# Optimization experiments

Hardware: AMD Instinct MI355X
Metric: run time of the kernel (lower is better)

The kernel has to match this reference:

```python
import jax, jax.numpy as jnp
import numpy as np

E, W, D = 50000, 6, 512
NH = 8
HD = D // NH
EPS = 1e-6


def setup_inputs() -> dict:
    key = jax.random.key(0)
    ks = jax.random.split(key, 12)
    s = 1.0 / np.sqrt(D)
    s2 = 1.0 / np.sqrt(D // 2)
    return {
        "h_i": jax.random.normal(ks[0], (E, D), jnp.float32),
        "evo_j": jax.random.normal(ks[1], (E, W, D), jnp.float32),
        "var_i": jax.random.uniform(ks[2], (E, D), jnp.float32),
        "var_j": jax.random.uniform(ks[3], (E, D), jnp.float32),
        "Wq": jax.random.normal(ks[4], (D, D), jnp.float32) * s,
        "bq": jnp.zeros((D,), jnp.float32),
        "Wk": jax.random.normal(ks[5], (D, D), jnp.float32) * s,
        "bk": jnp.zeros((D,), jnp.float32),
        "Wv": jax.random.normal(ks[6], (D, D), jnp.float32) * s,
        "bv": jnp.zeros((D,), jnp.float32),
        "log_decay": jnp.asarray(-2.0, jnp.float32),
        "W1": jax.random.normal(ks[7], (D, D // 2), jnp.float32) * s,
        "b1": jnp.zeros((D // 2,), jnp.float32),
        "W2": jax.random.normal(ks[8], (D // 2, 1), jnp.float32) * s2,
        "b2": jnp.zeros((1,), jnp.float32),
    }


def reference(h_i, evo_j, var_i, var_j, Wq, bq, Wk, bk, Wv, bv, log_decay, W1, b1, W2, b2):
    E_, W_, D_ = evo_j.shape
    scale = HD ** (-0.5)
    # projections: [E, nh, hd] and [E, W, nh, hd]
    Q = (h_i @ Wq + bq).reshape(E_, NH, HD)
    K = (evo_j @ Wk + bk).reshape(E_, W_, NH, HD)
    V = (evo_j @ Wv + bv).reshape(E_, W_, NH, HD)
    # windowed attention scores [E, nh, W]
    scores = jnp.einsum("ehd,ewhd->ehw", Q, K) * scale
    steps = jnp.arange(W_, dtype=jnp.float32)
    decay_w = jnp.exp(jnp.exp(log_decay) * steps)
    scores = scores + (decay_w / decay_w.sum())[None, None, :]
    attn = jax.nn.softmax(scores, axis=-1)
    # pool V over the window: [E, nh, hd] -> [E, D]
    pooled = jnp.einsum("ehw,ewhd->ehd", attn, V).reshape(E_, D_)
    # trust head: Linear -> GELU(exact) -> Linear
    hmid = jax.nn.gelu(pooled @ W1 + b1, approximate=False)
    trust_logit = (hmid @ W2 + b2)[:, 0]
    conf_i = 1.0 / (1.0 + jnp.maximum(jnp.sqrt(var_i.mean(-1)), EPS))
    conf_j = 1.0 / (1.0 + jnp.maximum(jnp.sqrt(var_j.mean(-1)), EPS))
    conf = jnp.sqrt(conf_i * conf_j)
    return jax.nn.sigmoid(trust_logit + jnp.maximum(jnp.log(conf), -5.0))
```

## Files before the change

kernel.cpp:

```cpp
#include <hip/hip_runtime.h>
#include <hip/hip_fp16.h>

typedef _Float16 f16;
typedef _Float16 f16x8 __attribute__((ext_vector_type(8)));
typedef __fp16 fp16x2_raw __attribute__((ext_vector_type(2)));
typedef float f32x4 __attribute__((ext_vector_type(4)));

#define DD 512
#define BM 32
#define WW 6
#define NH 8
#define QS 520
#define ES 136
#define EMAX 50000

union F16x8 { f16x8 v; unsigned u[4]; uint2 u2[2]; };
union H2U { __half2 h; unsigned u; };
union U4H { uint4 q; __half2 h[4]; };

__device__ __forceinline__ unsigned pkrtz(float a, float b) {
  union { fp16x2_raw h; unsigned u; } c;
  c.h = __builtin_amdgcn_cvt_pkrtz(a, b);
  return c.u;
}
__device__ __forceinline__ unsigned short f2h(float x) {
  union { f16 h; unsigned short u; } c; c.h = (f16)x; return c.u;
}
__device__ __forceinline__ float gelu_fast(float x) {
  float u = __expf(1.5957691216f * (x + 0.044715f * x * x * x));
  return x * u / (u + 1.f);
}
#define SCHED_FENCE() __builtin_amdgcn_sched_barrier(0)

__global__ void k_prep_qv(const float* __restrict__ src, unsigned short* __restrict__ dst) {
  int i = blockIdx.x * 256 + threadIdx.x;
  int j0 = (i & 1) * 4;
  int lane = (i >> 1) & 63;
  int kst = (i >> 7) & 15;
  int ct = (i >> 11) & 3;
  int wv = (i >> 13) & 7;
  int col = wv * 64 + ct * 16 + (lane & 15);
  int row = kst * 32 + (lane >> 4) * 8 + j0;
  ushort4 o;
  o.x = f2h(src[(size_t)(row + 0) * DD + col]);
  o.y = f2h(src[(size_t)(row + 1) * DD + col]);
  o.z = f2h(src[(size_t)(row + 2) * DD + col]);
  o.w = f2h(src[(size_t)(row + 3) * DD + col]);
  *(ushort4*)&dst[(size_t)(((wv * 4 + ct) * 16 + kst) * 64 + lane) * 8 + j0] = o;
}

__global__ void k_prep_wk(const float* __restrict__ src, unsigned short* __restrict__ dst) {
  int i = blockIdx.x * 256 + threadIdx.x;
  int j0 = (i & 1) * 4;
  int lane = (i >> 1) & 63;
  int ab = (i >> 7) & 1;
  int kst = (i >> 8) & 1;
  int ch = (i >> 9) & 15;
  int wv = (i >> 13) & 7;
  int row = ch * 32 + ab * 16 + (lane & 15);
  int cb = wv * 64 + kst * 32 + (j0 ? 16 : 0) + ((lane >> 4) & 3) * 4;
  float4 v = *(const float4*)&src[(size_t)row * DD + cb];
  ushort4 o; o.x = f2h(v.x); o.y = f2h(v.y); o.z = f2h(v.z); o.w = f2h(v.w);
  *(ushort4*)&dst[(size_t)((((wv * 16 + ch) * 2 + kst) * 2 + ab) * 64 + lane) * 8 + j0] = o;
}

__global__ void k_prep_w1(const float* __restrict__ src, unsigned short* __restrict__ dst) {
  int i = blockIdx.x * 256 + threadIdx.x;
  int j0 = (i & 1) * 4;
  int lane = (i >> 1) & 63;
  int kst = (i >> 7) & 15;
  int ct = (i >> 11) & 1;
  int wv = (i >> 12) & 7;
  int col = wv * 32 + ct * 16 + (lane & 15);
  int row = kst * 32 + (lane >> 4) * 8 + j0;
  ushort4 o;
  o.x = f2h(src[(size_t)(row + 0) * 256 + col]);
  o.y = f2h(src[(size_t)(row + 1) * 256 + col]);
  o.z = f2h(src[(size_t)(row + 2) * 256 + col]);
  o.w = f2h(src[(size_t)(row + 3) * 256 + col]);
  *(ushort4*)&dst[(size_t)(((wv * 2 + ct) * 16 + kst) * 64 + lane) * 8 + j0] = o;
}

__global__ __launch_bounds__(512, 4) void trust_main(
    const float* __restrict__ h_i, const float* __restrict__ evo,
    const float* __restrict__ var_i, const float* __restrict__ var_j,
    const float* __restrict__ bq, const float* __restrict__ bk, const float* __restrict__ bv,
    const float* __restrict__ ld, const float* __restrict__ b1,
    const float* __restrict__ W2, const float* __restrict__ b2,
    const unsigned short* __restrict__ wqA, const unsigned short* __restrict__ wkA,
    const unsigned short* __restrict__ wvA, const unsigned short* __restrict__ w1A,
    float* __restrict__ out) {
  __shared__ unsigned short buf_s[192 * ES];
  __shared__ float score_s[NH * BM * WW];
  __shared__ float logit_s[BM * NH];
  __shared__ float conf_s[BM];

  unsigned short* qh_s = buf_s;
  unsigned short* evo_s = buf_s;

  const int t = threadIdx.x;
  const int wv = t >> 6;
  const int l = t & 63;
  const int l16 = l & 15;
  const int lq = l >> 4;
  const int e0 = blockIdx.x * BM;
  const int row6 = e0 * 6;

  const float4* evb = (const float4*)evo;

  {
    const float4* h4 = (const float4*)h_i;
    #pragma unroll 4
    for (int i = 0; i < 8; ++i) {
      int idx = i * 512 + t;
      int row = idx >> 7, c4 = idx & 127;
      int ee = e0 + row; if (ee > EMAX - 1) ee = EMAX - 1;
      float4 v = h4[(size_t)ee * 128 + c4];
      uint2 o; o.x = pkrtz(v.x, v.y); o.y = pkrtz(v.z, v.w);
      *(uint2*)&qh_s[row * QS + c4 * 4] = o;
    }
    int ce = t >> 4, cs = t & 15;
    int ee = e0 + ce; if (ee > EMAX - 1) ee = EMAX - 1;
    const float4* vi4 = (const float4*)var_i + (size_t)ee * 128;
    const float4* vj4 = (const float4*)var_j + (size_t)ee * 128;
    float si = 0.f, sj = 0.f;
    #pragma unroll 4
    for (int i = 0; i < 8; ++i) {
      float4 a = vi4[i * 16 + cs]; si += a.x + a.y + a.z + a.w;
      float4 b = vj4[i * 16 + cs]; sj += b.x + b.y + b.z + b.w;
    }
    #pragma unroll
    for (int m = 1; m <= 8; m <<= 1) { si += __shfl_xor(si, m); sj += __shfl_xor(sj, m); }
    if (cs == 0) {
      float ci = 1.f / (1.f + fmaxf(sqrtf(si * (1.f / DD)), 1e-6f));
      float cj = 1.f / (1.f + fmaxf(sqrtf(sj * (1.f / DD)), 1e-6f));
      conf_s[ce] = fmaxf(0.5f * (__logf(ci) + __logf(cj)), -5.0f);
    }
  }
  __syncthreads();
  SCHED_FENCE();

  F16x8 qfrA[2], qfrB[2];
  float qbA, qbB;
  {
    f32x4 qaccA[4] = {}, qaccB[4] = {};
    const unsigned short* wqp = wqA + (size_t)wv * 4 * 16 * 512 + l * 8;
    #pragma unroll 2
    for (int kst = 0; kst < 16; ++kst) {
      f16x8 hbA = *reinterpret_cast<const f16x8*>(&qh_s[l16 * QS + kst * 32 + lq * 8]);
      f16x8 hbB = *reinterpret_cast<const f16x8*>(&qh_s[(16 + l16) * QS + kst * 32 + lq * 8]);
      #pragma unroll
      for (int ct = 0; ct < 4; ++ct) {
        f16x8 a = *reinterpret_cast<const f16x8*>(&wqp[(ct * 16 + kst) * 512]);
        qaccA[ct] = __builtin_amdgcn_mfma_f32_16x16x32_f16(a, hbA, qaccA[ct], 0, 0, 0);
        qaccB[ct] = __builtin_amdgcn_mfma_f32_16x16x32_f16(a, hbB, qaccB[ct], 0, 0, 0);
      }
    }
    qbA = 0.f; qbB = 0.f;
    #pragma unroll
    for (int ct = 0; ct < 4; ++ct) {
      float4 bq4 = *(const float4*)&bq[wv * 64 + ct * 16 + lq * 4];
      float4 bk4 = *(const float4*)&bk[wv * 64 + ct * 16 + lq * 4];
      {
        float q0 = qaccA[ct][0] + bq4.x, q1 = qaccA[ct][1] + bq4.y;
        float q2 = qaccA[ct][2] + bq4.z, q3 = qaccA[ct][3] + bq4.w;
        qbA += q0 * bk4.x + q1 * bk4.y + q2 * bk4.z + q3 * bk4.w;
        qfrA[ct >> 1].u[(ct & 1) * 2]     = pkrtz(q0, q1);
        qfrA[ct >> 1].u[(ct & 1) * 2 + 1] = pkrtz(q2, q3);
      }
      {
        float q0 = qaccB[ct][0] + bq4.x, q1 = qaccB[ct][1] + bq4.y;
        float q2 = qaccB[ct][2] + bq4.z, q3 = qaccB[ct][3] + bq4.w;
        qbB += q0 * bk4.x + q1 * bk4.y + q2 * bk4.z + q3 * bk4.w;
        qfrB[ct >> 1].u[(ct & 1) * 2]     = pkrtz(q0, q1);
        qfrB[ct >> 1].u[(ct & 1) * 2 + 1] = pkrtz(q2, q3);
      }
    }
    qbA += __shfl_xor(qbA, 16); qbA += __shfl_xor(qbA, 32);
    qbB += __shfl_xor(qbB, 16); qbB += __shfl_xor(qbB, 32);
  }
  SCHED_FENCE();

  f32x4 sA0 = {}, sA1 = {}, sA2 = {}, sA3 = {}, sA4 = {}, sA5 = {};
  f32x4 sB0 = {}, sB1 = {}, sB2 = {}, sB3 = {}, sB4 = {}, sB5 = {};
  const unsigned short* wkp = wkA + (size_t)wv * 16 * 2 * 2 * 512 + l * 8;
  const unsigned short* wvp = wvA + (size_t)wv * 4 * 16 * 512 + l * 8;

  #pragma unroll 1
  for (int q = 0; q < 4; ++q) {
    __syncthreads();
    #pragma unroll 4
    for (int i = 0; i < 12; ++i) {
      int idx = i * 512 + t;
      int row = idx >> 5, c4 = idx & 31;
      int gr = row6 + row; if (gr > EMAX * 6 - 1) gr = EMAX * 6 - 1;
      float4 v = evb[(size_t)gr * 128 + q * 32 + c4];
      uint2 o; o.x = pkrtz(v.x, v.y); o.y = pkrtz(v.z, v.w);
      *(uint2*)&evo_s[row * ES + c4 * 4] = o;
    }
    __syncthreads();
    #pragma unroll 1
    for (int ci = 0; ci < 4; ++ci) {
      int ch = q * 4 + ci;
      F16x8 a00, a01, a10, a11;
      a00.v = *reinterpret_cast<const f16x8*>(&wkp[((ch * 2 + 0) * 2 + 0) * 512]);
      a01.v = *reinterpret_cast<const f16x8*>(&wkp[((ch * 2 + 0) * 2 + 1) * 512]);
      a10.v = *reinterpret_cast<const f16x8*>(&wkp[((ch * 2 + 1) * 2 + 0) * 512]);
      a11.v = *reinterpret_cast<const f16x8*>(&wkp[((ch * 2 + 1) * 2 + 1) * 512]);
      SCHED_FENCE();
      f32x4 qkA0 = {}, qkA1 = {}, qkB0 = {}, qkB1 = {};
      qkA0 = __builtin_amdgcn_mfma_f32_16x16x32_f16(a00.v, qfrA[0].v, qkA0, 0, 0, 0);
      qkA1 = __builtin_amdgcn_mfma_f32_16x16x32_f16(a01.v, qfrA[0].v, qkA1, 0, 0, 0);
      qkB0 = __builtin_amdgcn_mfma_f32_16x16x32_f16(a00.v, qfrB[0].v, qkB0, 0, 0, 0);
      qkB1 = __builtin_amdgcn_mfma_f32_16x16x32_f16(a01.v, qfrB[0].v, qkB1, 0, 0, 0);
      qkA0 = __builtin_amdgcn_mfma_f32_16x16x32_f16(a10.v, qfrA[1].v, qkA0, 0, 0, 0);
      qkA1 = __builtin_amdgcn_mfma_f32_16x16x32_f16(a11.v, qfrA[1].v, qkA1, 0, 0, 0);
      qkB0 = __builtin_amdgcn_mfma_f32_16x16x32_f16(a10.v, qfrB[1].v, qkB0, 0, 0, 0);
      qkB1 = __builtin_amdgcn_mfma_f32_16x16x32_f16(a11.v, qfrB[1].v, qkB1, 0, 0, 0);
      F16x8 afA, afB;
      afA.u[0] = pkrtz(qkA0[0], qkA0[1]); afA.u[1] = pkrtz(qkA0[2], qkA0[3]);
      afA.u[2] = pkrtz(qkA1[0], qkA1[1]); afA.u[3] = pkrtz(qkA1[2], qkA1[3]);
      afB.u[0] = pkrtz(qkB0[0], qkB0[1]); afB.u[1] = pkrtz(qkB0[2], qkB0[3]);
      afB.u[2] = pkrtz(qkB1[0], qkB1[1]); afB.u[3] = pkrtz(qkB1[2], qkB1[3]);
      int cb = ci * 32 + lq * 4;
      F16x8 b;
      b.u2[0] = *(const uint2*)&evo_s[(0 * 16 + l16) * ES + cb];
      b.u2[1] = *(const uint2*)&evo_s[(0 * 16 + l16) * ES + cb + 16];
      sA0 = __builtin_amdgcn_mfma_f32_16x16x32_f16(afA.v, b.v, sA0, 0, 0, 0);
      b.u2[0] = *(const uint2*)&evo_s[(1 * 16 + l16) * ES + cb];
      b.u2[1] = *(const uint2*)&evo_s[(1 * 16 + l16) * ES + cb + 16];
      sA1 = __builtin_amdgcn_mfma_f32_16x16x32_f16(afA.v, b.v, sA1, 0, 0, 0);
      b.u2[0] = *(const uint2*)&evo_s[(2 * 16 + l16) * ES + cb];
      b.u2[1] = *(const uint2*)&evo_s[(2 * 16 + l16) * ES + cb + 16];
      sA2 = __builtin_amdgcn_mfma_f32_16x16x32_f16(afA.v, b.v, sA2, 0, 0, 0);
      b.u2[0] = *(const uint2*)&evo_s[(3 * 16 + l16) * ES + cb];
      b.u2[1] = *(const uint2*)&evo_s[(3 * 16 + l16) * ES + cb + 16];
      sA3 = __builtin_amdgcn_mfma_f32_16x16x32_f16(afA.v, b.v, sA3, 0, 0, 0);
      b.u2[0] = *(const uint2*)&evo_s[(4 * 16 + l16) * ES + cb];
      b.u2[1] = *(const uint2*)&evo_s[(4 * 16 + l16) * ES + cb + 16];
      sA4 = __builtin_amdgcn_mfma_f32_16x16x32_f16(afA.v, b.v, sA4, 0, 0, 0);
      b.u2[0] = *(const uint2*)&evo_s[(5 * 16 + l16) * ES + cb];
      b.u2[1] = *(const uint2*)&evo_s[(5 * 16 + l16) * ES + cb + 16];
      sA5 = __builtin_amdgcn_mfma_f32_16x16x32_f16(afA.v, b.v, sA5, 0, 0, 0);
      b.u2[0] = *(const uint2*)&evo_s[(6 * 16 + l16) * ES + cb];
      b.u2[1] = *(const uint2*)&evo_s[(6 * 16 + l16) * ES + cb + 16];
      sB0 = __builtin_amdgcn_mfma_f32_16x16x32_f16(afB.v, b.v, sB0, 0, 0, 0);
      b.u2[0] = *(const uint2*)&evo_s[(7 * 16 + l16) * ES + cb];
      b.u2[1] = *(const uint2*)&evo_s[(7 * 16 + l16) * ES + cb + 16];
      sB1 = __builtin_amdgcn_mfma_f32_16x16x32_f16(afB.v, b.v, sB1, 0, 0, 0);
      b.u2[0] = *(const uint2*)&evo_s[(8 * 16 + l16) * ES + cb];
      b.u2[1] = *(const uint2*)&evo_s[(8 * 16 + l16) * ES + cb + 16];
      sB2 = __builtin_amdgcn_mfma_f32_16x16x32_f16(afB.v, b.v, sB2, 0, 0, 0);
      b.u2[0] = *(const uint2*)&evo_s[(9 * 16 + l16) * ES + cb];
      b.u2[1] = *(const uint2*)&evo_s[(9 * 16 + l16) * ES + cb + 16];
      sB3 = __builtin_amdgcn_mfma_f32_16x16x32_f16(afB.v, b.v, sB3, 0, 0, 0);
      b.u2[0] = *(const uint2*)&evo_s[(10 * 16 + l16) * ES + cb];
      b.u2[1] = *(const uint2*)&evo_s[(10 * 16 + l16) * ES + cb + 16];
      sB4 = __builtin_amdgcn_mfma_f32_16x16x32_f16(afB.v, b.v, sB4, 0, 0, 0);
      b.u2[0] = *(const uint2*)&evo_s[(11 * 16 + l16) * ES + cb];
      b.u2[1] = *(const uint2*)&evo_s[(11 * 16 + l16) * ES + cb + 16];
      sB5 = __builtin_amdgcn_mfma_f32_16x16x32_f16(afB.v, b.v, sB5, 0, 0, 0);
    }
  }
  SCHED_FENCE();

  #pragma unroll
  for (int r = 0; r < 4; ++r) {
    int e = lq * 4 + r;
    int base = l16 - 6 * e;
    { int w = base;      if (w >= 0 && w < WW) { score_s[wv * 192 + e * 6 + w] = sA0[r];
                                                score_s[wv * 192 + (16 + e) * 6 + w] = sB0[r]; } }
    { int w = base + 16; if (w >= 0 && w < WW) { score_s[wv * 192 + e * 6 + w] = sA1[r];
                                                score_s[wv * 192 + (16 + e) * 6 + w] = sB1[r]; } }
    { int w = base + 32; if (w >= 0 && w < WW) { score_s[wv * 192 + e * 6 + w] = sA2[r];
                                                score_s[wv * 192 + (16 + e) * 6 + w] = sB2[r]; } }
    { int w = base + 48; if (w >= 0 && w < WW) { score_s[wv * 192 + e * 6 + w] = sA3[r];
                                                score_s[wv * 192 + (16 + e) * 6 + w] = sB3[r]; } }
    { int w = base + 64; if (w >= 0 && w < WW) { score_s[wv * 192 + e * 6 + w] = sA4[r];
                                                score_s[wv * 192 + (16 + e) * 6 + w] = sB4[r]; } }
    { int w = base + 80; if (w >= 0 && w < WW) { score_s[wv * 192 + e * 6 + w] = sA5[r];
                                                score_s[wv * 192 + (16 + e) * 6 + w] = sB5[r]; } }
  }
  float biasw[WW];
  {
    float rd = __expf(ld[0]);
    float dsum = 0.f;
    #pragma unroll
    for (int w6 = 0; w6 < WW; ++w6) { biasw[w6] = __expf(rd * (float)w6); dsum += biasw[w6]; }
    float dinv = 1.f / dsum;
    #pragma unroll
    for (int w6 = 0; w6 < WW; ++w6) biasw[w6] *= dinv;
  }
  #pragma unroll
  for (int r = 0; r < 4; ++r) {
    int e = lq * 4 + r;
    float qbvA = __shfl(qbA, e);
    float qbvB = __shfl(qbB, e);
    float scA[WW], scB[WW]; float mxA = -1e30f, mxB = -1e30f;
    #pragma unroll
    for (int w6 = 0; w6 < WW; ++w6) {
      scA[w6] = 0.125f * (score_s[wv * 192 + e * 6 + w6] + qbvA) + biasw[w6];
      scB[w6] = 0.125f * (score_s[wv * 192 + (16 + e) * 6 + w6] + qbvB) + biasw[w6];
      mxA = fmaxf(mxA, scA[w6]); mxB = fmaxf(mxB, scB[w6]);
    }
    float ssA = 0.f, ssB = 0.f;
    #pragma unroll
    for (int w6 = 0; w6 < WW; ++w6) {
      scA[w6] = __expf(scA[w6] - mxA); ssA += scA[w6];
      scB[w6] = __expf(scB[w6] - mxB); ssB += scB[w6];
    }
    float siA = 1.f / ssA, siB = 1.f / ssB;
    if (l16 == 0) {
      #pragma unroll
      for (int w6 = 0; w6 < WW; ++w6) {
        score_s[wv * 192 + e * 6 + w6] = scA[w6] * siA;
        score_s[wv * 192 + (16 + e) * 6 + w6] = scB[w6] * siB;
      }
    }
  }
  SCHED_FENCE();

  f32x4 paccA[4] = {}, paccB[4] = {};
  {
    __half2 aw2A[WW], aw2B[WW];
    #pragma unroll
    for (int w6 = 0; w6 < WW; ++w6) {
      float vA = score_s[wv * 192 + l16 * 6 + w6];
      float vB = score_s[wv * 192 + (16 + l16) * 6 + w6];
      H2U a; a.u = pkrtz(vA, vA); aw2A[w6] = a.h;
      H2U c; c.u = pkrtz(vB, vB); aw2B[w6] = c.h;
    }
    const int arowA = l16 * 6, arowB = 96 + l16 * 6;
    #pragma unroll 1
    for (int q = 3; q >= 0; --q) {
      if (q != 3) {
        __syncthreads();
        #pragma unroll 4
        for (int i = 0; i < 12; ++i) {
          int idx = i * 512 + t;
          int row = idx >> 5, c4 = idx & 31;
          int gr = row6 + row; if (gr > EMAX * 6 - 1) gr = EMAX * 6 - 1;
          float4 v = evb[(size_t)gr * 128 + q * 32 + c4];
          uint2 o; o.x = pkrtz(v.x, v.y); o.y = pkrtz(v.z, v.w);
          *(uint2*)&evo_s[row * ES + c4 * 4] = o;
        }
        __syncthreads();
      }
      F16x8 v0, v1, v2, v3, nv0, nv1, nv2, nv3;
      v0.v = *reinterpret_cast<const f16x8*>(&wvp[(0 * 16 + q * 4) * 512]);
      v1.v = *reinterpret_cast<const f16x8*>(&wvp[(1 * 16 + q * 4) * 512]);
      v2.v = *reinterpret_cast<const f16x8*>(&wvp[(2 * 16 + q * 4) * 512]);
      v3.v = *reinterpret_cast<const f16x8*>(&wvp[(3 * 16 + q * 4) * 512]);
      #pragma unroll 1
      for (int ci = 0; ci < 4; ++ci) {
        int nc = q * 4 + ((ci + 1) & 3);
        nv0.v = *reinterpret_cast<const f16x8*>(&wvp[(0 * 16 + nc) * 512]);
        nv1.v = *reinterpret_cast<const f16x8*>(&wvp[(1 * 16 + nc) * 512]);
        nv2.v = *reinterpret_cast<const f16x8*>(&wvp[(2 * 16 + nc) * 512]);
        nv3.v = *reinterpret_cast<const f16x8*>(&wvp[(3 * 16 + nc) * 512]);
        SCHED_FENCE();
        H2U z; z.u = 0;
        __half2 aA0 = z.h, aA1 = z.h, aA2 = z.h, aA3 = z.h;
        __half2 aB0 = z.h, aB1 = z.h, aB2 = z.h, aB3 = z.h;
        #pragma unroll
        for (int w6 = 0; w6 < WW; ++w6) {
          U4H vv; vv.q = *(const uint4*)&evo_s[(arowA + w6) * ES + ci * 32 + lq * 8];
          aA0 = __hfma2(vv.h[0], aw2A[w6], aA0);
          aA1 = __hfma2(vv.h[1], aw2A[w6], aA1);
          aA2 = __hfma2(vv.h[2], aw2A[w6], aA2);
          aA3 = __hfma2(vv.h[3], aw2A[w6], aA3);
        }
        #pragma unroll
        for (int w6 = 0; w6 < WW; ++w6) {
          U4H vv; vv.q = *(const uint4*)&evo_s[(arowB + w6) * ES + ci * 32 + lq * 8];
          aB0 = __hfma2(vv.h[0], aw2B[w6], aB0);
          aB1 = __hfma2(vv.h[1], aw2B[w6], aB1);
          aB2 = __hfma2(vv.h[2], aw2B[w6], aB2);
          aB3 = __hfma2(vv.h[3], aw2B[w6], aB3);
        }
        F16x8 afA, afB;
        { H2U c; c.h = aA0; afA.u[0] = c.u; c.h = aA1; afA.u[1] = c.u;
          c.h = aA2; afA.u[2] = c.u; c.h = aA3; afA.u[3] = c.u;
          c.h = aB0; afB.u[0] = c.u; c.h = aB1; afB.u[1] = c.u;
          c.h = aB2; afB.u[2] = c.u; c.h = aB3; afB.u[3] = c.u; }
        paccA[0] = __builtin_amdgcn_mfma_f32_16x16x32_f16(afA.v, v0.v, paccA[0], 0, 0, 0);
        paccB[0] = __builtin_amdgcn_mfma_f32_16x16x32_f16(afB.v, v0.v, paccB[0], 0, 0, 0);
        paccA[1] = __builtin_amdgcn_mfma_f32_16x16x32_f16(afA.v, v1.v, paccA[1], 0, 0, 0);
        paccB[1] = __builtin_amdgcn_mfma_f32_16x16x32_f16(afB.v, v1.v, paccB[1], 0, 0, 0);
        paccA[2] = __builtin_amdgcn_mfma_f32_16x16x32_f16(afA.v, v2.v, paccA[2], 0, 0, 0);
        paccB[2] = __builtin_amdgcn_mfma_f32_16x16x32_f16(afB.v, v2.v, paccB[2], 0, 0, 0);
        paccA[3] = __builtin_amdgcn_mfma_f32_16x16x32_f16(afA.v, v3.v, paccA[3], 0, 0, 0);
        paccB[3] = __builtin_amdgcn_mfma_f32_16x16x32_f16(afB.v, v3.v, paccB[3], 0, 0, 0);
        v0 = nv0; v1 = nv1; v2 = nv2; v3 = nv3;
      }
    }
  }

  __syncthreads();
  #pragma unroll
  for (int ct = 0; ct < 4; ++ct) {
    int col = wv * 64 + ct * 16 + l16;
    float bvv = bv[col];
    #pragma unroll
    for (int r = 0; r < 4; ++r) {
      qh_s[(lq * 4 + r) * QS + col] = f2h(paccA[ct][r] + bvv);
      qh_s[(16 + lq * 4 + r) * QS + col] = f2h(paccB[ct][r] + bvv);
    }
  }
  __syncthreads();

  {
    f32x4 haccA[2] = {}, haccB[2] = {};
    const unsigned short* w1p = w1A + (size_t)wv * 2 * 16 * 512 + l * 8;
    #pragma unroll 2
    for (int kst = 0; kst < 16; ++kst) {
      f16x8 aA = *reinterpret_cast<const f16x8*>(&qh_s[l16 * QS + kst * 32 + lq * 8]);
      f16x8 aB = *reinterpret_cast<const f16x8*>(&qh_s[(16 + l16) * QS + kst * 32 + lq * 8]);
      #pragma unroll
      for (int ct = 0; ct < 2; ++ct) {
        f16x8 b = *reinterpret_cast<const f16x8*>(&w1p[(ct * 16 + kst) * 512]);
        haccA[ct] = __builtin_amdgcn_mfma_f32_16x16x32_f16(aA, b, haccA[ct], 0, 0, 0);
        haccB[ct] = __builtin_amdgcn_mfma_f32_16x16x32_f16(aB, b, haccB[ct], 0, 0, 0);
      }
    }
    float lgA[4] = {0.f, 0.f, 0.f, 0.f}, lgB[4] = {0.f, 0.f, 0.f, 0.f};
    #pragma unroll
    for (int ct = 0; ct < 2; ++ct) {
      int m = wv * 32 + ct * 16 + l16;
      float b1v = b1[m], w2v = W2[m];
      #pragma unroll
      for (int r = 0; r < 4; ++r) {
        lgA[r] += gelu_fast(haccA[ct][r] + b1v) * w2v;
        lgB[r] += gelu_fast(haccB[ct][r] + b1v) * w2v;
      }
    }
    #pragma unroll
    for (int r = 0; r < 4; ++r) {
      #pragma unroll
      for (int m = 1; m <= 8; m <<= 1) {
        lgA[r] += __shfl_xor(lgA[r], m);
        lgB[r] += __shfl_xor(lgB[r], m);
      }
    }
    if (l16 == 0) {
      #pragma unroll
      for (int r = 0; r < 4; ++r) {
        logit_s[(lq * 4 + r) * NH + wv] = lgA[r];
        logit_s[(16 + lq * 4 + r) * NH + wv] = lgB[r];
      }
    }
  }
  __syncthreads();

  if (t < BM) {
    int ee = e0 + t;
    if (ee < EMAX) {
      float s = 0.f;
      #pragma unroll
      for (int w8 = 0; w8 < NH; ++w8) s += logit_s[t * NH + w8];
      s += b2[0] + conf_s[t];
      out[ee] = 1.f / (1.f + __expf(-s));
    }
  }
}

extern "C" void kernel_launch(void* const* d_in, const int* in_sizes, int n_in,
                              void* d_out, int out_size, void* d_ws, size_t ws_size,
                              hipStream_t stream) {
  (void)in_sizes; (void)n_in; (void)out_size; (void)ws_size;
  const float* h_i = (const float*)d_in[0];
  const float* evo = (const float*)d_in[1];
  const float* vi  = (const float*)d_in[2];
  const float* vj  = (const float*)d_in[3];
  const float* Wq  = (const float*)d_in[4];
  const float* bq  = (const float*)d_in[5];
  const float* Wk  = (const float*)d_in[6];
  const float* bk  = (const float*)d_in[7];
  const float* Wv  = (const float*)d_in[8];
  const float* bv  = (const float*)d_in[9];
  const float* ld  = (const float*)d_in[10];
  const float* W1  = (const float*)d_in[11];
  const float* b1  = (const float*)d_in[12];
  const float* W2  = (const float*)d_in[13];
  const float* b2  = (const float*)d_in[14];
  float* out = (float*)d_out;

  unsigned short* ws  = (unsigned short*)d_ws;
  unsigned short* wqA = ws;
  unsigned short* wkA = ws + 262144;
  unsigned short* wvA = ws + 524288;
  unsigned short* w1A = ws + 786432;

  k_prep_qv<<<256, 256, 0, stream>>>(Wq, wqA);
  k_prep_wk<<<256, 256, 0, stream>>>(Wk, wkA);
  k_prep_qv<<<256, 256, 0, stream>>>(Wv, wvA);
  k_prep_w1<<<128, 256, 0, stream>>>(W1, w1A);
  trust_main<<<1563, 512, 0, stream>>>(h_i, evo, vi, vj, bq, bk, bv, ld, b1, W2, b2,
                                       wqA, wkA, wvA, w1A, out);
}
```

Before: 365.3 us.

## Read evo_j directly from global in V pooling instead of staging through LDS

The attention-weighted pooling of V now loads evo_j rows straight from global memory into registers and accumulates in fp32. This replaces the per-quarter LDS staging loop and its two __syncthreads, and it also drops the software prefetch of Wv fragments. The aim is to remove LDS round-trips and barriers. The cost is uncoalesced, per-lane global reads that may go to L2/HBM again if the evo_j data is no longer cached, along with more register pressure from the fp32 accumulators.

New measurement: 1.060 ms. +190.1%, slower.

```diff
diff --git a/kernel.cpp b/kernel.cpp
--- a/kernel.cpp
+++ b/kernel.cpp
@@ -322,67 +322,51 @@
 
   f32x4 paccA[4] = {}, paccB[4] = {};
   {
-    __half2 aw2A[WW], aw2B[WW];
+    float awA[WW], awB[WW];
     #pragma unroll
     for (int w6 = 0; w6 < WW; ++w6) {
-      float vA = score_s[wv * 192 + l16 * 6 + w6];
-      float vB = score_s[wv * 192 + (16 + l16) * 6 + w6];
-      H2U a; a.u = pkrtz(vA, vA); aw2A[w6] = a.h;
-      H2U c; c.u = pkrtz(vB, vB); aw2B[w6] = c.h;
-    }
-    const int arowA = l16 * 6, arowB = 96 + l16 * 6;
+      awA[w6] = score_s[wv * 192 + l16 * 6 + w6];
+      awB[w6] = score_s[wv * 192 + (16 + l16) * 6 + w6];
+    }
+    const size_t grA0 = (size_t)(row6 + l16 * 6);
+    int eB = e0 + 16 + l16; if (eB > EMAX - 1) eB = EMAX - 1;
+    const size_t grB0 = (size_t)eB * 6;
     #pragma unroll 1
-    for (int q = 3; q >= 0; --q) {
-      if (q != 3) {
-        __syncthreads();
-        #pragma unroll 4
-        for (int i = 0; i < 12; ++i) {
-          int idx = i * 512 + t;
-          int row = idx >> 5, c4 = idx & 31;
-          int gr = row6 + row; if (gr > EMAX * 6 - 1) gr = EMAX * 6 - 1;
-          float4 v = evb[(size_t)gr * 128 + q * 32 + c4];
-          uint2 o; o.x = pkrtz(v.x, v.y); o.y = pkrtz(v.z, v.w);
-          *(uint2*)&evo_s[row * ES + c4 * 4] = o;
-        }
-        __syncthreads();
-      }
-      F16x8 v0, v1, v2, v3, nv0, nv1, nv2, nv3;
-      v0.v = *reinterpret_cast<const f16x8*>(&wvp[(0 * 16 + q * 4) * 512]);
-      v1.v = *reinterpret_cast<const f16x8*>(&wvp[(1 * 16 + q * 4) * 512]);
-      v2.v = *reinterpret_cast<const f16x8*>(&wvp[(2 * 16 + q * 4) * 512]);
-      v3.v = *reinterpret_cast<const f16x8*>(&wvp[(3 * 16 + q * 4) * 512]);
+    for (int q = 0; q < 4; ++q) {
       #pragma unroll 1
       for (int ci = 0; ci < 4; ++ci) {
-        int nc = q * 4 + ((ci + 1) & 3);
-        nv0.v = *reinterpret_cast<const f16x8*>(&wvp[(0 * 16 + nc) * 512]);
-        nv1.v = *reinterpret_cast<const f16x8*>(&wvp[(1 * 16 + nc) * 512]);
-        nv2.v = *reinterpret_cast<const f16x8*>(&wvp[(2 * 16 + nc) * 512]);
-        nv3.v = *reinterpret_cast<const f16x8*>(&wvp[(3 * 16 + nc) * 512]);
-        SCHED_FENCE();
-        H2U z; z.u = 0;
-        __half2 aA0 = z.h, aA1 = z.h, aA2 = z.h, aA3 = z.h;
-        __half2 aB0 = z.h, aB1 = z.h, aB2 = z.h, aB3 = z.h;
+        int ch = q * 4 + ci;
+        F16x8 v0, v1, v2, v3;
+        v0.v = *reinterpret_cast<const f16x8*>(&wvp[(0 * 16 + ch) * 512]);
+        v1.v = *reinterpret_cast<const f16x8*>(&wvp[(1 * 16 + ch) * 512]);
+        v2.v = *reinterpret_cast<const f16x8*>(&wvp[(2 * 16 + ch) * 512]);
+        v3.v = *reinterpret_cast<const f16x8*>(&wvp[(3 * 16 + ch) * 512]);
+        int c4 = q * 32 + ci * 8 + lq * 2;
+        float aA0 = 0.f, aA1 = 0.f, aA2 = 0.f, aA3 = 0.f, aA4 = 0.f, aA5 = 0.f, aA6 = 0.f, aA7 = 0.f;
         #pragma unroll
         for (int w6 = 0; w6 < WW; ++w6) {
-          U4H vv; vv.q = *(const uint4*)&evo_s[(arowA + w6) * ES + ci * 32 + lq * 8];
-          aA0 = __hfma2(vv.h[0], aw2A[w6], aA0);
-          aA1 = __hfma2(vv.h[1], aw2A[w6], aA1);
-          aA2 = __hfma2(vv.h[2], aw2A[w6], aA2);
-          aA3 = __hfma2(vv.h[3], aw2A[w6], aA3);
+          const float4* p = &evb[(grA0 + w6) * 128 + c4];
+          float4 x = p[0], y = p[1];
+          float aw = awA[w6];
+          aA0 += aw * x.x; aA1 += aw * x.y; aA2 += aw * x.z; aA3 += aw * x.w;
+          aA4 += aw * y.x; aA5 += aw * y.y; aA6 += aw * y.z; aA7 += aw * y.w;
         }
+        SCHED_FENCE();
+        float aB0 = 0.f, aB1 = 0.f, aB2 = 0.f, aB3 = 0.f, aB4 = 0.f, aB5 = 0.f, aB6 = 0.f, aB7 = 0.f;
         #pragma unroll
         for (int w6 = 0; w6 < WW; ++w6) {
-          U4H vv; vv.q = *(const uint4*)&evo_s[(arowB + w6) * ES + ci * 32 + lq * 8];
-          aB0 = __hfma2(vv.h[0], aw2B[w6], aB0);
-          aB1 = __hfma2(vv.h[1], aw2B[w6], aB1);
-          aB2 = __hfma2(vv.h[2], aw2B[w6], aB2);
-          aB3 = __hfma2(vv.h[3], aw2B[w6], aB3);
+          const float4* p = &evb[(grB0 + w6) * 128 + c4];
+          float4 x = p[0], y = p[1];
+          float aw = awB[w6];
+          aB0 += aw * x.x; aB1 += aw * x.y; aB2 += aw * x.z; aB3 += aw * x.w;
+          aB4 += aw * y.x; aB5 += aw * y.y; aB6 += aw * y.z; aB7 += aw * y.w;
         }
+        SCHED_FENCE();
         F16x8 afA, afB;
-        { H2U c; c.h = aA0; afA.u[0] = c.u; c.h = aA1; afA.u[1] = c.u;
-          c.h = aA2; afA.u[2] = c.u; c.h = aA3; afA.u[3] = c.u;
-          c.h = aB0; afB.u[0] = c.u; c.h = aB1; afB.u[1] = c.u;
-          c.h = aB2; afB.u[2] = c.u; c.h = aB3; afB.u[3] = c.u; }
+        afA.u[0] = pkrtz(aA0, aA1); afA.u[1] = pkrtz(aA2, aA3);
+        afA.u[2] = pkrtz(aA4, aA5); afA.u[3] = pkrtz(aA6, aA7);
+        afB.u[0] = pkrtz(aB0, aB1); afB.u[1] = pkrtz(aB2, aB3);
+        afB.u[2] = pkrtz(aB4, aB5); afB.u[3] = pkrtz(aB6, aB7);
         paccA[0] = __builtin_amdgcn_mfma_f32_16x16x32_f16(afA.v, v0.v, paccA[0], 0, 0, 0);
         paccB[0] = __builtin_amdgcn_mfma_f32_16x16x32_f16(afB.v, v0.v, paccB[0], 0, 0, 0);
         paccA[1] = __builtin_amdgcn_mfma_f32_16x16x32_f16(afA.v, v1.v, paccA[1], 0, 0, 0);
@@ -391,7 +375,6 @@
         paccB[2] = __builtin_amdgcn_mfma_f32_16x16x32_f16(afB.v, v2.v, paccB[2], 0, 0, 0);
         paccA[3] = __builtin_amdgcn_mfma_f32_16x16x32_f16(afA.v, v3.v, paccA[3], 0, 0, 0);
         paccB[3] = __builtin_amdgcn_mfma_f32_16x16x32_f16(afB.v, v3.v, paccB[3], 0, 0, 0);
-        v0 = nv0; v1 = nv1; v2 = nv2; v3 = nv3;
       }
     }
   }
```
